# Kernel tuning notes

Measured on AMD Instinct MI355X. Metric: run time of the kernel, lower is better.

The kernel has to match this reference:

```python
import jax, jax.numpy as jnp
import numpy as np

NUM_HEADS = 16
HEAD_SIZE = 64
N_EMBD = 1024


def setup_inputs() -> dict:
    key = jax.random.key(0)
    ks = jax.random.split(key, 7)
    B, T, S, C, H, D = 4, 1024, 1024, N_EMBD, NUM_HEADS, HEAD_SIZE
    s = 1.0 / np.sqrt(C)
    return {
        "x": jax.random.normal(ks[0], (B, T, C), jnp.float32),
        "y_enc": jax.random.normal(ks[1], (B, S, C), jnp.float32),
        # stacked per-head projection weights [H, C, D]
        "Wq": jax.random.normal(ks[2], (H, C, D), jnp.float32) * s,
        "Wk": jax.random.normal(ks[3], (H, C, D), jnp.float32) * s,
        "Wv": jax.random.normal(ks[4], (H, C, D), jnp.float32) * s,
        "Wo": jax.random.normal(ks[5], (C, C), jnp.float32) * s,
        "bo": jax.random.normal(ks[6], (C,), jnp.float32) * 0.01,
    }


def reference(x, y_enc, Wq, Wk, Wv, Wo, bo):
    B, T, C = x.shape
    # per-head projections (batched over heads)
    q = jnp.einsum("btc,hcd->bhtd", x, Wq)       # [B,H,T,D]
    k = jnp.einsum("bsc,hcd->bhsd", y_enc, Wk)   # [B,H,S,D]
    v = jnp.einsum("bsc,hcd->bhsd", y_enc, Wv)   # [B,H,S,D]
    # NOTE: original scales by C**-0.5 with C = n_embd (full embed dim)
    scale = C ** (-0.5)
    wei = jnp.einsum("bhtd,bhsd->bhts", q, k) * scale
    wei = jax.nn.softmax(wei, axis=-1)
    out = jnp.einsum("bhts,bhsd->bhtd", wei, v)  # [B,H,T,D]
    # concat heads along last dim == transpose + reshape
    out = out.transpose(0, 2, 1, 3).reshape(B, T, -1)  # [B,T,H*D]
    return out @ Wo.T + bo
```

## Files before the change

### kernel.cpp

```cpp
#include <hip/hip_runtime.h>
#include <hip/hip_bf16.h>

using u16 = unsigned short;
typedef short bf16x8 __attribute__((ext_vector_type(8)));
typedef float f32x4 __attribute__((ext_vector_type(4)));
typedef u16 u16x8 __attribute__((ext_vector_type(8)));
typedef u16 u16x4 __attribute__((ext_vector_type(4)));

#define B_ 4
#define T_ 1024
#define S_ 1024
#define C_ 1024
#define H_ 16
#define D_ 64
#define SCALE_LOG2E 0.0450842200f

#define AKSTR 40
#define KSTR  72

__device__ __forceinline__ u16 f2bf(float f) {
    __hip_bfloat16 h = __float2bfloat16(f);
    u16 u; __builtin_memcpy(&u, &h, 2); return u;
}
__device__ __forceinline__ float bf2f(u16 u) {
    __hip_bfloat16 h; __builtin_memcpy(&h, &u, 2);
    return __bfloat162float(h);
}

__global__ __launch_bounds__(256) void prep_kernel(const float* __restrict__ x,
                                                   const float* __restrict__ yenc,
                                                   const float* __restrict__ Wq,
                                                   const float* __restrict__ Wk,
                                                   const float* __restrict__ Wv,
                                                   const float* __restrict__ Wo,
                                                   u16* __restrict__ xbf,
                                                   u16* __restrict__ ybf,
                                                   u16* __restrict__ wtq,
                                                   u16* __restrict__ wtk,
                                                   u16* __restrict__ wtv,
                                                   u16* __restrict__ wohi,
                                                   u16* __restrict__ wolo) {
    const int z = blockIdx.z;
    const int t = threadIdx.x;
    if (z < 3) {
        __shared__ float ldsT[64][65];
        const float* W = (z == 0) ? Wq : (z == 1) ? Wk : Wv;
        u16* Wt = (z == 0) ? wtq : (z == 1) ? wtk : wtv;
        const int c0 = blockIdx.x * 64;
        const int h  = blockIdx.y;
        const float* Wh = W + (size_t)h * C_ * D_;
        u16* Wth = Wt + (size_t)h * D_ * C_;
        {
            int c = t >> 2;
            int d0 = (t & 3) * 16;
            #pragma unroll
            for (int q = 0; q < 4; ++q) {
                float4 v = *reinterpret_cast<const float4*>(Wh + (size_t)(c0 + c) * D_ + d0 + q * 4);
                ldsT[d0 + q * 4 + 0][c] = v.x;
                ldsT[d0 + q * 4 + 1][c] = v.y;
                ldsT[d0 + q * 4 + 2][c] = v.z;
                ldsT[d0 + q * 4 + 3][c] = v.w;
            }
        }
        __syncthreads();
        {
            int d = t >> 2;
            int cq = (t & 3) * 16;
            u16x8 o0, o1;
            #pragma unroll
            for (int j = 0; j < 8; ++j) o0[j] = f2bf(ldsT[d][cq + j]);
            #pragma unroll
            for (int j = 0; j < 8; ++j) o1[j] = f2bf(ldsT[d][cq + 8 + j]);
            *reinterpret_cast<u16x8*>(Wth + (size_t)d * C_ + c0 + cq) = o0;
            *reinterpret_cast<u16x8*>(Wth + (size_t)d * C_ + c0 + cq + 8) = o1;
        }
    } else if (z == 3) {
        int bid = blockIdx.y * 16 + blockIdx.x;
        #pragma unroll
        for (int it = 0; it < 4; ++it) {
            int i = (bid * 4 + it) * 256 + t;
            float4 v = reinterpret_cast<const float4*>(Wo)[i];
            float vv[4] = {v.x, v.y, v.z, v.w};
            u16x4 hh, ll;
            #pragma unroll
            for (int j = 0; j < 4; ++j) {
                u16 hb = f2bf(vv[j]);
                hh[j] = hb;
                ll[j] = f2bf(vv[j] - bf2f(hb));
            }
            reinterpret_cast<u16x4*>(wohi)[i] = hh;
            reinterpret_cast<u16x4*>(wolo)[i] = ll;
        }
    } else {
        const float* src = (z == 4) ? x : yenc;
        u16* dst = (z == 4) ? xbf : ybf;
        int bid = blockIdx.y * 16 + blockIdx.x;
        #pragma unroll
        for (int it = 0; it < 16; ++it) {
            int i = (bid * 16 + it) * 256 + t;
            float4 v = reinterpret_cast<const float4*>(src)[i];
            u16x4 o;
            o[0] = f2bf(v.x); o[1] = f2bf(v.y); o[2] = f2bf(v.z); o[3] = f2bf(v.w);
            reinterpret_cast<u16x4*>(dst)[i] = o;
        }
    }
}

__global__ __launch_bounds__(256) void proj_mfma_kernel(const u16* __restrict__ xbf,
                                                        const u16* __restrict__ ybf,
                                                        const u16* __restrict__ wtq,
                                                        const u16* __restrict__ wtk,
                                                        const u16* __restrict__ wtv,
                                                        u16* __restrict__ qb,
                                                        u16* __restrict__ kb,
                                                        u16* __restrict__ vtb) {
    __shared__ __align__(16) u16 Al[128 * AKSTR];
    __shared__ __align__(16) u16 Bl[128 * AKSTR];

    const int z = blockIdx.z;
    const u16* Xb = (z == 0) ? xbf : ybf;
    const u16* Wt = (z == 0) ? wtq : (z == 1) ? wtk : wtv;
    u16* out      = (z == 0) ? qb  : (z == 1) ? kb  : vtb;
    const bool transposed = (z == 2);

    const int n0  = blockIdx.x * 128;
    const int i0  = blockIdx.y * 128;
    const int tid = threadIdx.x;
    const int lane = tid & 63, w = tid >> 6;
    const int g = lane >> 4, li = lane & 15;
    const int wm = (w >> 1) * 64, wn = (w & 1) * 64;
    const int ar = tid >> 1, ac = (tid & 1) * 16;

    f32x4 acc[4][4] = {};

    for (int k0 = 0; k0 < C_; k0 += 32) {
        __syncthreads();
        {
            const u16* sa = Xb + (size_t)(i0 + ar) * C_ + k0 + ac;
            *reinterpret_cast<u16x8*>(&Al[ar * AKSTR + ac])     = *reinterpret_cast<const u16x8*>(sa);
            *reinterpret_cast<u16x8*>(&Al[ar * AKSTR + ac + 8]) = *reinterpret_cast<const u16x8*>(sa + 8);
            const u16* sb = Wt + (size_t)(n0 + ar) * C_ + k0 + ac;
            *reinterpret_cast<u16x8*>(&Bl[ar * AKSTR + ac])     = *reinterpret_cast<const u16x8*>(sb);
            *reinterpret_cast<u16x8*>(&Bl[ar * AKSTR + ac + 8]) = *reinterpret_cast<const u16x8*>(sb + 8);
        }
        __syncthreads();

        bf16x8 a[4], b[4];
        #pragma unroll
        for (int mf = 0; mf < 4; ++mf)
            a[mf] = *reinterpret_cast<const bf16x8*>(&Al[(wm + mf * 16 + li) * AKSTR + g * 8]);
        #pragma unroll
        for (int nf = 0; nf < 4; ++nf)
            b[nf] = *reinterpret_cast<const bf16x8*>(&Bl[(wn + nf * 16 + li) * AKSTR + g * 8]);
        #pragma unroll
        for (int mf = 0; mf < 4; ++mf)
            #pragma unroll
            for (int nf = 0; nf < 4; ++nf)
                acc[mf][nf] = __builtin_amdgcn_mfma_f32_16x16x32_bf16(a[mf], b[nf], acc[mf][nf], 0, 0, 0);
    }

    if (!transposed) {
        #pragma unroll
        for (int mf = 0; mf < 4; ++mf) {
            int gi = i0 + wm + mf * 16 + g * 4;
            #pragma unroll
            for (int r = 0; r < 4; ++r) {
                int m = gi + r;
                int b = m >> 10, tt = m & 1023;
                #pragma unroll
                for (int nf = 0; nf < 4; ++nf) {
                    int n = n0 + wn + nf * 16 + li;
                    int h = n >> 6, d = n & 63;
                    out[(((size_t)(b * H_ + h) * T_) + tt) * D_ + d] = f2bf(acc[mf][nf][r]);
                }
            }
        }
    } else {
        #pragma unroll
        for (int mf = 0; mf < 4; ++mf) {
            int gi = i0 + wm + mf * 16 + g * 4;
            int b = gi >> 10, s = gi & 1023;
            #pragma unroll
            for (int nf = 0; nf < 4; ++nf) {
                int n = n0 + wn + nf * 16 + li;
                int h = n >> 6, d = n & 63;
                u16x4 o;
                #pragma unroll
                for (int r = 0; r < 4; ++r) o[r] = f2bf(acc[mf][nf][r]);
                *reinterpret_cast<u16x4*>(out + (((size_t)(b * H_ + h) * D_) + d) * S_ + s) = o;
            }
        }
    }
}

__global__ __launch_bounds__(512) void attn_mfma_kernel(const u16* __restrict__ Q,
                                                        const u16* __restrict__ K,
                                                        const u16* __restrict__ Vt,
                                                        u16* __restrict__ out_hi,
                                                        u16* __restrict__ out_lo) {
    __shared__ __align__(16) u16 Kl[64 * KSTR];
    __shared__ __align__(16) u16 Vl[64 * KSTR];
    __shared__ __align__(16) u16 Pl[8][16 * KSTR];

    const int t0  = blockIdx.x * 128;
    const int h   = blockIdx.y;
    const int b   = blockIdx.z;
    const int tid = threadIdx.x;
    const int lane = tid & 63, w = tid >> 6;
    const int g = lane >> 4, li = lane & 15;

    const size_t bh = (size_t)(b * H_ + h);
    const u16* Qp = Q  + bh * T_ * D_;
    const u16* Kp = K  + bh * S_ * D_;
    const u16* Vp = Vt + bh * D_ * S_;

    bf16x8 qf[2];
    #pragma unroll
    for (int ks = 0; ks < 2; ++ks)
        qf[ks] = *reinterpret_cast<const bf16x8*>(
            Qp + (size_t)(t0 + w * 16 + li) * D_ + ks * 32 + g * 8);

    const int sr = tid >> 3, sc = (tid & 7) * 8;

    float lsum[4] = {};
    f32x4 accO[4] = {};

    for (int s0 = 0; s0 < S_; s0 += 64) {
        __syncthreads();
        *reinterpret_cast<u16x8*>(&Kl[sr * KSTR + sc]) =
            *reinterpret_cast<const u16x8*>(Kp + (size_t)(s0 + sr) * D_ + sc);
        *reinterpret_cast<u16x8*>(&Vl[sr * KSTR + sc]) =
            *reinterpret_cast<const u16x8*>(Vp + (size_t)sr * S_ + s0 + sc);
        __syncthreads();

        f32x4 scf[4] = {};
        #pragma unroll
        for (int nf = 0; nf < 4; ++nf)
            #pragma unroll
            for (int ks = 0; ks < 2; ++ks) {
                bf16x8 kf = *reinterpret_cast<const bf16x8*>(
                    &Kl[(nf * 16 + li) * KSTR + ks * 32 + g * 8]);
                scf[nf] = __builtin_amdgcn_mfma_f32_16x16x32_bf16(qf[ks], kf, scf[nf], 0, 0, 0);
            }

        u16* Pw = Pl[w];
        #pragma unroll
        for (int nf = 0; nf < 4; ++nf)
            #pragma unroll
            for (int r = 0; r < 4; ++r) {
                float p = exp2f(scf[nf][r] * SCALE_LOG2E);
                lsum[r] += p;
                Pw[(g * 4 + r) * KSTR + nf * 16 + li] = f2bf(p);
            }

        bf16x8 pf[2];
        #pragma unroll
        for (int ks = 0; ks < 2; ++ks)
            pf[ks] = *reinterpret_cast<const bf16x8*>(&Pl[w][li * KSTR + ks * 32 + g * 8]);

        #pragma unroll
        for (int nf = 0; nf < 4; ++nf)
            #pragma unroll
            for (int ks = 0; ks < 2; ++ks) {
                bf16x8 vf = *reinterpret_cast<const bf16x8*>(
                    &Vl[(nf * 16 + li) * KSTR + ks * 32 + g * 8]);
                accO[nf] = __builtin_amdgcn_mfma_f32_16x16x32_bf16(pf[ks], vf, accO[nf], 0, 0, 0);
            }
    }

    #pragma unroll
    for (int r = 0; r < 4; ++r) {
        #pragma unroll
        for (int off = 1; off < 16; off <<= 1)
            lsum[r] += __shfl_xor(lsum[r], off, 64);
    }

    #pragma unroll
    for (int r = 0; r < 4; ++r) {
        float inv = 1.0f / lsum[r];
        int tt = t0 + w * 16 + g * 4 + r;
        u16* dh = out_hi + ((size_t)(b * T_) + tt) * C_ + h * D_;
        u16* dl = out_lo + ((size_t)(b * T_) + tt) * C_ + h * D_;
        #pragma unroll
        for (int nf = 0; nf < 4; ++nf) {
            float v = accO[nf][r] * inv;
            u16 hb = f2bf(v);
            dh[nf * 16 + li] = hb;
            dl[nf * 16 + li] = f2bf(v - bf2f(hb));
        }
    }
}

__global__ __launch_bounds__(512) void outproj_mfma_kernel(const u16* __restrict__ Ahi,
                                                           const u16* __restrict__ Alo,
                                                           const u16* __restrict__ Bhi,
                                                           const u16* __restrict__ Blo,
                                                           const float* __restrict__ bo,
                                                           float* __restrict__ out) {
    __shared__ __align__(16) u16 AH[128 * AKSTR];
    __shared__ __align__(16) u16 AL[128 * AKSTR];
    __shared__ __align__(16) u16 BH[128 * AKSTR];
    __shared__ __align__(16) u16 BL[128 * AKSTR];

    const int n0  = blockIdx.x * 128;
    const int i0  = blockIdx.y * 128;
    const int tid = threadIdx.x;
    const int lane = tid & 63, w = tid >> 6;
    const int g = lane >> 4, li = lane & 15;
    const int wm = (w >> 2) * 64, wn = (w & 3) * 32;
    const int ar = tid >> 2, ac = (tid & 3) * 8;

    f32x4 acc[4][2] = {};

    for (int k0 = 0; k0 < C_; k0 += 32) {
        __syncthreads();
        {
            *reinterpret_cast<u16x8*>(&AH[ar * AKSTR + ac]) =
                *reinterpret_cast<const u16x8*>(Ahi + (size_t)(i0 + ar) * C_ + k0 + ac);
            *reinterpret_cast<u16x8*>(&AL[ar * AKSTR + ac]) =
                *reinterpret_cast<const u16x8*>(Alo + (size_t)(i0 + ar) * C_ + k0 + ac);
            *reinterpret_cast<u16x8*>(&BH[ar * AKSTR + ac]) =
                *reinterpret_cast<const u16x8*>(Bhi + (size_t)(n0 + ar) * C_ + k0 + ac);
            *reinterpret_cast<u16x8*>(&BL[ar * AKSTR + ac]) =
                *reinterpret_cast<const u16x8*>(Blo + (size_t)(n0 + ar) * C_ + k0 + ac);
        }
        __syncthreads();

        bf16x8 ah[4], al[4], bh[2], bl[2];
        #pragma unroll
        for (int mf = 0; mf < 4; ++mf) {
            ah[mf] = *reinterpret_cast<const bf16x8*>(&AH[(wm + mf * 16 + li) * AKSTR + g * 8]);
            al[mf] = *reinterpret_cast<const bf16x8*>(&AL[(wm + mf * 16 + li) * AKSTR + g * 8]);
        }
        #pragma unroll
        for (int nf = 0; nf < 2; ++nf) {
            bh[nf] = *reinterpret_cast<const bf16x8*>(&BH[(wn + nf * 16 + li) * AKSTR + g * 8]);
            bl[nf] = *reinterpret_cast<const bf16x8*>(&BL[(wn + nf * 16 + li) * AKSTR + g * 8]);
        }
        #pragma unroll
        for (int mf = 0; mf < 4; ++mf)
            #pragma unroll
            for (int nf = 0; nf < 2; ++nf) {
                acc[mf][nf] = __builtin_amdgcn_mfma_f32_16x16x32_bf16(ah[mf], bh[nf], acc[mf][nf], 0, 0, 0);
                acc[mf][nf] = __builtin_amdgcn_mfma_f32_16x16x32_bf16(ah[mf], bl[nf], acc[mf][nf], 0, 0, 0);
                acc[mf][nf] = __builtin_amdgcn_mfma_f32_16x16x32_bf16(al[mf], bh[nf], acc[mf][nf], 0, 0, 0);
            }
    }

    float bj[2];
    #pragma unroll
    for (int nf = 0; nf < 2; ++nf) bj[nf] = bo[n0 + wn + nf * 16 + li];
    #pragma unroll
    for (int mf = 0; mf < 4; ++mf) {
        int row = i0 + wm + mf * 16 + g * 4;
        #pragma unroll
        for (int r = 0; r < 4; ++r)
            #pragma unroll
            for (int nf = 0; nf < 2; ++nf)
                out[(size_t)(row + r) * C_ + n0 + wn + nf * 16 + li] = acc[mf][nf][r] + bj[nf];
    }
}

extern "C" void kernel_launch(void* const* d_in, const int* in_sizes, int n_in,
                              void* d_out, int out_size, void* d_ws, size_t ws_size,
                              hipStream_t stream) {
    const float* x    = (const float*)d_in[0];
    const float* yenc = (const float*)d_in[1];
    const float* Wq   = (const float*)d_in[2];
    const float* Wk   = (const float*)d_in[3];
    const float* Wv   = (const float*)d_in[4];
    const float* Wo   = (const float*)d_in[5];
    const float* bo   = (const float*)d_in[6];
    float* out = (float*)d_out;

    char* ws = (char*)d_ws;
    const size_t MB = 1024 * 1024;
    u16* xbf   = (u16*)(ws + 0 * MB);
    u16* ybf   = (u16*)(ws + 8 * MB);
    u16* wtq   = (u16*)(ws + 16 * MB);
    u16* wtk   = (u16*)(ws + 18 * MB);
    u16* wtv   = (u16*)(ws + 20 * MB);
    u16* wohi  = (u16*)(ws + 22 * MB);
    u16* wolo  = (u16*)(ws + 24 * MB);
    u16* qb    = (u16*)(ws + 26 * MB);
    u16* kb    = (u16*)(ws + 34 * MB);
    u16* vtb   = (u16*)(ws + 42 * MB);
    u16* ahi   = xbf;
    u16* alo   = ybf;

    prep_kernel<<<dim3(16, 16, 6), 256, 0, stream>>>(x, yenc, Wq, Wk, Wv, Wo,
                                                     xbf, ybf, wtq, wtk, wtv, wohi, wolo);

    proj_mfma_kernel<<<dim3(8, 32, 3), 256, 0, stream>>>(xbf, ybf, wtq, wtk, wtv, qb, kb, vtb);

    attn_mfma_kernel<<<dim3(T_ / 128, H_, B_), 512, 0, stream>>>(qb, kb, vtb, ahi, alo);

    outproj_mfma_kernel<<<dim3(8, 32), 512, 0, stream>>>(ahi, alo, wohi, wolo, bo, out);
}
```

Baseline: 231.2 us.

## Double-buffer LDS tiles with register prefetch in projection GEMMs; retile out-proj

Both the QKV projection and output projection GEMMs now keep two LDS buffers. Each iteration loads the next K-slice from global into registers while MFMAs run on the current buffer, then stores it to the other buffer, which removes one barrier per iteration and hides global load latency. The output projection also moves from 512-thread 128x128 tiles to 256-thread 128x64 tiles, doubling the grid to 512 blocks. The cost is more LDS and registers per block, which may reduce occupancy.

```diff
diff --git a/kernel.cpp b/kernel.cpp
--- a/kernel.cpp
+++ b/kernel.cpp
@@ -26,6 +26,9 @@
     __hip_bfloat16 h; __builtin_memcpy(&h, &u, 2);
     return __bfloat162float(h);
 }
+__device__ __forceinline__ u16x8 ldg8(const u16* p) { return *reinterpret_cast<const u16x8*>(p); }
+__device__ __forceinline__ void sts8(u16* p, u16x8 v) { *reinterpret_cast<u16x8*>(p) = v; }
+__device__ __forceinline__ bf16x8 lds8(const u16* p) { return *reinterpret_cast<const bf16x8*>(p); }
 
 __global__ __launch_bounds__(256) void prep_kernel(const float* __restrict__ x,
                                                    const float* __restrict__ yenc,
@@ -114,8 +117,8 @@
                                                         u16* __restrict__ qb,
                                                         u16* __restrict__ kb,
                                                         u16* __restrict__ vtb) {
-    __shared__ __align__(16) u16 Al[128 * AKSTR];
-    __shared__ __align__(16) u16 Bl[128 * AKSTR];
+    __shared__ __align__(16) u16 Al[2][128 * AKSTR];
+    __shared__ __align__(16) u16 Bl[2][128 * AKSTR];
 
     const int z = blockIdx.z;
     const u16* Xb = (z == 0) ? xbf : ybf;
@@ -131,32 +134,49 @@
     const int wm = (w >> 1) * 64, wn = (w & 1) * 64;
     const int ar = tid >> 1, ac = (tid & 1) * 16;
 
+    const u16* aSrc = Xb + (size_t)(i0 + ar) * C_ + ac;
+    const u16* bSrc = Wt + (size_t)(n0 + ar) * C_ + ac;
+
+    u16x8 ra0 = ldg8(aSrc), ra1 = ldg8(aSrc + 8);
+    u16x8 rb0 = ldg8(bSrc), rb1 = ldg8(bSrc + 8);
+    sts8(&Al[0][ar * AKSTR + ac], ra0);
+    sts8(&Al[0][ar * AKSTR + ac + 8], ra1);
+    sts8(&Bl[0][ar * AKSTR + ac], rb0);
+    sts8(&Bl[0][ar * AKSTR + ac + 8], rb1);
+    __syncthreads();
+
     f32x4 acc[4][4] = {};
-
+    int cur = 0;
     for (int k0 = 0; k0 < C_; k0 += 32) {
-        __syncthreads();
-        {
-            const u16* sa = Xb + (size_t)(i0 + ar) * C_ + k0 + ac;
-            *reinterpret_cast<u16x8*>(&Al[ar * AKSTR + ac])     = *reinterpret_cast<const u16x8*>(sa);
-            *reinterpret_cast<u16x8*>(&Al[ar * AKSTR + ac + 8]) = *reinterpret_cast<const u16x8*>(sa + 8);
-            const u16* sb = Wt + (size_t)(n0 + ar) * C_ + k0 + ac;
-            *reinterpret_cast<u16x8*>(&Bl[ar * AKSTR + ac])     = *reinterpret_cast<const u16x8*>(sb);
-            *reinterpret_cast<u16x8*>(&Bl[ar * AKSTR + ac + 8]) = *reinterpret_cast<const u16x8*>(sb + 8);
-        }
-        __syncthreads();
+        const bool has_next = (k0 + 32 < C_);
+        if (has_next) {
+            ra0 = ldg8(aSrc + k0 + 32);
+            ra1 = ldg8(aSrc + k0 + 40);
+            rb0 = ldg8(bSrc + k0 + 32);
+            rb1 = ldg8(bSrc + k0 + 40);
+        }
 
         bf16x8 a[4], b[4];
         #pragma unroll
         for (int mf = 0; mf < 4; ++mf)
-            a[mf] = *reinterpret_cast<const bf16x8*>(&Al[(wm + mf * 16 + li) * AKSTR + g * 8]);
+            a[mf] = lds8(&Al[cur][(wm + mf * 16 + li) * AKSTR + g * 8]);
         #pragma unroll
         for (int nf = 0; nf < 4; ++nf)
-            b[nf] = *reinterpret_cast<const bf16x8*>(&Bl[(wn + nf * 16 + li) * AKSTR + g * 8]);
+            b[nf] = lds8(&Bl[cur][(wn + nf * 16 + li) * AKSTR + g * 8]);
         #pragma unroll
         for (int mf = 0; mf < 4; ++mf)
             #pragma unroll
             for (int nf = 0; nf < 4; ++nf)
                 acc[mf][nf] = __builtin_amdgcn_mfma_f32_16x16x32_bf16(a[mf], b[nf], acc[mf][nf], 0, 0, 0);
+
+        if (has_next) {
+            sts8(&Al[cur ^ 1][ar * AKSTR + ac], ra0);
+            sts8(&Al[cur ^ 1][ar * AKSTR + ac + 8], ra1);
+            sts8(&Bl[cur ^ 1][ar * AKSTR + ac], rb0);
+            sts8(&Bl[cur ^ 1][ar * AKSTR + ac + 8], rb1);
+        }
+        __syncthreads();
+        cur ^= 1;
     }
 
     if (!transposed) {
@@ -291,51 +311,65 @@
     }
 }
 
-__global__ __launch_bounds__(512) void outproj_mfma_kernel(const u16* __restrict__ Ahi,
+__global__ __launch_bounds__(256) void outproj_mfma_kernel(const u16* __restrict__ Ahi,
                                                            const u16* __restrict__ Alo,
                                                            const u16* __restrict__ Bhi,
                                                            const u16* __restrict__ Blo,
                                                            const float* __restrict__ bo,
                                                            float* __restrict__ out) {
-    __shared__ __align__(16) u16 AH[128 * AKSTR];
-    __shared__ __align__(16) u16 AL[128 * AKSTR];
-    __shared__ __align__(16) u16 BH[128 * AKSTR];
-    __shared__ __align__(16) u16 BL[128 * AKSTR];
-
-    const int n0  = blockIdx.x * 128;
+    __shared__ __align__(16) u16 AH[2][128 * AKSTR];
+    __shared__ __align__(16) u16 AL[2][128 * AKSTR];
+    __shared__ __align__(16) u16 BH[2][64 * AKSTR];
+    __shared__ __align__(16) u16 BL[2][64 * AKSTR];
+
+    const int n0  = blockIdx.x * 64;
     const int i0  = blockIdx.y * 128;
     const int tid = threadIdx.x;
     const int lane = tid & 63, w = tid >> 6;
     const int g = lane >> 4, li = lane & 15;
-    const int wm = (w >> 2) * 64, wn = (w & 3) * 32;
-    const int ar = tid >> 2, ac = (tid & 3) * 8;
+    const int wm = (w >> 1) * 64, wn = (w & 1) * 32;
+    const int ar = tid >> 1, ac = (tid & 1) * 16;
+    const int br = tid >> 2, bc = (tid & 3) * 8;
+
+    const u16* ahSrc = Ahi + (size_t)(i0 + ar) * C_ + ac;
+    const u16* alSrc = Alo + (size_t)(i0 + ar) * C_ + ac;
+    const u16* bhSrc = Bhi + (size_t)(n0 + br) * C_ + bc;
+    const u16* blSrc = Blo + (size_t)(n0 + br) * C_ + bc;
+
+    u16x8 rh0 = ldg8(ahSrc), rh1 = ldg8(ahSrc + 8);
+    u16x8 rl0 = ldg8(alSrc), rl1 = ldg8(alSrc + 8);
+    u16x8 rbh = ldg8(bhSrc), rbl = ldg8(blSrc);
+    sts8(&AH[0][ar * AKSTR + ac], rh0);
+    sts8(&AH[0][ar * AKSTR + ac + 8], rh1);
+    sts8(&AL[0][ar * AKSTR + ac], rl0);
+    sts8(&AL[0][ar * AKSTR + ac + 8], rl1);
+    sts8(&BH[0][br * AKSTR + bc], rbh);
+    sts8(&BL[0][br * AKSTR + bc], rbl);
+    __syncthreads();
 
     f32x4 acc[4][2] = {};
-
+    int cur = 0;
     for (int k0 = 0; k0 < C_; k0 += 32) {
-        __syncthreads();
-        {
-            *reinterpret_cast<u16x8*>(&AH[ar * AKSTR + ac]) =
-                *reinterpret_cast<const u16x8*>(Ahi + (size_t)(i0 + ar) * C_ + k0 + ac);
-            *reinterpret_cast<u16x8*>(&AL[ar * AKSTR + ac]) =
-                *reinterpret_cast<const u16x8*>(Alo + (size_t)(i0 + ar) * C_ + k0 + ac);
-            *reinterpret_cast<u16x8*>(&BH[ar * AKSTR + ac]) =
-                *reinterpret_cast<const u16x8*>(Bhi + (size_t)(n0 + ar) * C_ + k0 + ac);
-            *reinterpret_cast<u16x8*>(&BL[ar * AKSTR + ac]) =
-                *reinterpret_cast<const u16x8*>(Blo + (size_t)(n0 + ar) * C_ + k0 + ac);
-        }
-        __syncthreads();
+        const bool has_next = (k0 + 32 < C_);
+        if (has_next) {
+            rh0 = ldg8(ahSrc + k0 + 32);
+            rh1 = ldg8(ahSrc + k0 + 40);
+            rl0 = ldg8(alSrc + k0 + 32);
+            rl1 = ldg8(alSrc + k0 + 40);
+            rbh = ldg8(bhSrc + k0 + 32);
+            rbl = ldg8(blSrc + k0 + 32);
+        }
 
         bf16x8 ah[4], al[4], bh[2], bl[2];
         #pragma unroll
         for (int mf = 0; mf < 4; ++mf) {
-            ah[mf] = *reinterpret_cast<const bf16x8*>(&AH[(wm + mf * 16 + li) * AKSTR + g * 8]);
-            al[mf] = *reinterpret_cast<const bf16x8*>(&AL[(wm + mf * 16 + li) * AKSTR + g * 8]);
+            ah[mf] = lds8(&AH[cur][(wm + mf * 16 + li) * AKSTR + g * 8]);
+            al[mf] = lds8(&AL[cur][(wm + mf * 16 + li) * AKSTR + g * 8]);
         }
         #pragma unroll
         for (int nf = 0; nf < 2; ++nf) {
-            bh[nf] = *reinterpret_cast<const bf16x8*>(&BH[(wn + nf * 16 + li) * AKSTR + g * 8]);
-            bl[nf] = *reinterpret_cast<const bf16x8*>(&BL[(wn + nf * 16 + li) * AKSTR + g * 8]);
+            bh[nf] = lds8(&BH[cur][(wn + nf * 16 + li) * AKSTR + g * 8]);
+            bl[nf] = lds8(&BL[cur][(wn + nf * 16 + li) * AKSTR + g * 8]);
         }
         #pragma unroll
         for (int mf = 0; mf < 4; ++mf)
@@ -345,6 +379,17 @@
                 acc[mf][nf] = __builtin_amdgcn_mfma_f32_16x16x32_bf16(ah[mf], bl[nf], acc[mf][nf], 0, 0, 0);
                 acc[mf][nf] = __builtin_amdgcn_mfma_f32_16x16x32_bf16(al[mf], bh[nf], acc[mf][nf], 0, 0, 0);
             }
+
+        if (has_next) {
+            sts8(&AH[cur ^ 1][ar * AKSTR + ac], rh0);
+            sts8(&AH[cur ^ 1][ar * AKSTR + ac + 8], rh1);
+            sts8(&AL[cur ^ 1][ar * AKSTR + ac], rl0);
+            sts8(&AL[cur ^ 1][ar * AKSTR + ac + 8], rl1);
+            sts8(&BH[cur ^ 1][br * AKSTR + bc], rbh);
+            sts8(&BL[cur ^ 1][br * AKSTR + bc], rbl);
+        }
+        __syncthreads();
+        cur ^= 1;
     }
 
     float bj[2];
@@ -395,5 +440,5 @@
 
     attn_mfma_kernel<<<dim3(T_ / 128, H_, B_), 512, 0, stream>>>(qb, kb, vtb, ahi, alo);
 
-    outproj_mfma_kernel<<<dim3(8, 32), 512, 0, stream>>>(ahi, alo, wohi, wolo, bo, out);
-}
+    outproj_mfma_kernel<<<dim3(16, 32), 256, 0, stream>>>(ahi, alo, wohi, wolo, bo, out);
+}
```

Measured after the change: 214.3 us. 1.08x faster.
